# Kernel optimization log

Measured on AMD Instinct MI355X. Metric: run time of the kernel, lower is better.

Reference implementation:

```python
import jax, jax.numpy as jnp
import numpy as np

LN_EPS = 1e-5  # torch LayerNorm default
EPS = 1e-8     # slot-attention eps

def _ln(x, g, b):
    m = jnp.mean(x, axis=-1, keepdims=True)
    v = jnp.mean(jnp.square(x - m), axis=-1, keepdims=True)
    return (x - m) * jax.lax.rsqrt(v + LN_EPS) * g + b

def setup_inputs() -> dict:
    key = jax.random.key(0)
    ks = jax.random.split(key, 16)
    b, d, n_s, h = 131072, 256, 16, 256
    w_scale = d ** -0.5
    return {
        "inputs": jax.random.normal(ks[0], (b, 1, d), jnp.float32),
        "noise": jax.random.normal(ks[1], (n_s, d), jnp.float32),
        "slots_mu": jax.random.normal(ks[2], (1, d), jnp.float32),
        "slots_sigma": jax.random.uniform(ks[3], (1, d), jnp.float32),
        "Wq": jax.random.normal(ks[4], (d, d), jnp.float32) * w_scale,
        "bq": jnp.zeros((d,), jnp.float32),
        "Wk": jax.random.normal(ks[5], (d, d), jnp.float32) * w_scale,
        "bk": jnp.zeros((d,), jnp.float32),
        "Wv": jax.random.normal(ks[6], (d, d), jnp.float32) * w_scale,
        "bv": jnp.zeros((d,), jnp.float32),
        "W_ih": jax.random.normal(ks[7], (3 * d, d), jnp.float32) * w_scale,
        "W_hh": jax.random.normal(ks[8], (3 * d, d), jnp.float32) * w_scale,
        "b_ih": jnp.zeros((3 * d,), jnp.float32),
        "b_hh": jnp.zeros((3 * d,), jnp.float32),
        "W1": jax.random.normal(ks[9], (h, d), jnp.float32) * w_scale,
        "b1": jnp.zeros((h,), jnp.float32),
        "W2": jax.random.normal(ks[10], (d, h), jnp.float32) * (h ** -0.5),
        "b2": jnp.zeros((d,), jnp.float32),
        "g_in": jnp.ones((d,), jnp.float32),
        "be_in": jnp.zeros((d,), jnp.float32),
        "g_s": jnp.ones((d,), jnp.float32),
        "be_s": jnp.zeros((d,), jnp.float32),
        "g_f": jnp.ones((d,), jnp.float32),
        "be_f": jnp.zeros((d,), jnp.float32),
    }

def reference(inputs, noise, slots_mu, slots_sigma, Wq, bq, Wk, bk, Wv, bv,
              W_ih, W_hh, b_ih, b_hh, W1, b1, W2, b2,
              g_in, be_in, g_s, be_s, g_f, be_f):
    b, w, d = inputs.shape  # w == 1 required by the module's LayerNorm(dim)
    x = inputs.reshape(b, w * d)
    scale = d ** -0.5
    iters = 3

    slots = slots_mu + slots_sigma * noise  # (n_s, d), reparameterized normal

    x = _ln(x, g_in, be_in)
    k = x @ Wk.T + bk  # (b, d)
    v = x @ Wv.T + bv  # (b, d)

    for _ in range(iters):
        slots_prev = slots
        s = _ln(slots, g_s, be_s)
        q = s @ Wq.T + bq                      # (n_s, d)
        dots = jnp.einsum('nd,bd->nb', q, k) * scale
        attn = jax.nn.softmax(dots, axis=0) + EPS   # softmax over slots
        attn = attn / jnp.sum(attn, axis=-1, keepdims=True)
        updates = jnp.einsum('bd,nb->nd', v, attn)  # (n_s, d)
        # torch GRUCell
        gx = updates @ W_ih.T + b_ih                # (n_s, 3d)
        gh = slots_prev @ W_hh.T + b_hh
        xr, xz, xn = jnp.split(gx, 3, axis=-1)
        hr, hz, hn = jnp.split(gh, 3, axis=-1)
        r = jax.nn.sigmoid(xr + hr)
        z = jax.nn.sigmoid(xz + hz)
        n = jnp.tanh(xn + r * hn)
        slots = (1.0 - z) * n + z * slots_prev
        ff = jax.nn.relu(_ln(slots, g_f, be_f) @ W1.T + b1) @ W2.T + b2
        slots = slots + ff
    return slots
```

## Files before the change

### kernel.cpp

```cpp
#include <hip/hip_runtime.h>
#include <stdint.h>

#define B_ROWS 131072
#define SCALE 0.0625f
#define LN_EPS 1e-5f
#define ATTN_EPS 1e-8f

#define BIG_BLOCKS 512
#define ROWS_PER_BLOCK (B_ROWS / BIG_BLOCKS)
#define ROWS_PER_WAVE  (ROWS_PER_BLOCK / 4)
#define NSLICE BIG_BLOCKS

#define WS_PARTU 0
#define WS_PARTS (WS_PARTU + NSLICE*4096)
#define WS_U     (WS_PARTS + NSLICE*16)
#define WS_S     (WS_U + 4096)
#define WS_SLOTS (WS_S + 64)
#define WS_MID   (WS_SLOTS + 4096)
#define WS_GX    (WS_MID + 4096)
#define WS_GH    (WS_GX + 12288)
#define WS_H1    (WS_GH + 12288)
#define WS_QKG   (WS_H1 + 4096)
#define WS_QB    (WS_QKG + 4096)
#define WS_WIHV  (WS_QB + 64)
#define WS_BGX   (WS_WIHV + 196608)
#define WS_WQKG  (WS_BGX + 768)
#define WS_U2G   (WS_WQKG + 65536)
#define WS_U1    (WS_U2G + 256)
#define WS_C1    (WS_U1 + 256)

__global__ __launch_bounds__(256) void k_pre1(
    const float* __restrict__ Wq, const float* __restrict__ bq,
    const float* __restrict__ Wk, const float* __restrict__ bk,
    const float* __restrict__ Wv, const float* __restrict__ bv,
    const float* __restrict__ W_ih, const float* __restrict__ b_ih,
    const float* __restrict__ g_in, const float* __restrict__ be_in,
    float* __restrict__ ws)
{
  int bid = blockIdx.x, t = threadIdx.x;
  if (bid < 48) {
    int j0 = bid * 16;
    float acc[16];
#pragma unroll
    for (int r = 0; r < 16; r++) acc[r] = 0.f;
    int d = t;
    for (int dd = 0; dd < 256; dd++) {
      float v = Wv[dd * 256 + d];
#pragma unroll
      for (int r = 0; r < 16; r++)
        acc[r] = fmaf(W_ih[(j0 + r) * 256 + dd], v, acc[r]);
    }
#pragma unroll
    for (int r = 0; r < 16; r++) ws[WS_WIHV + (j0 + r) * 256 + d] = acc[r];
    if (t < 16) {
      int j = j0 + t;
      float a = b_ih[j];
      for (int dd = 0; dd < 256; dd++)
        a = fmaf(W_ih[j * 256 + dd], bv[dd], a);
      ws[WS_BGX + j] = a;
    }
  } else if (bid < 80) {
    int c0 = (bid - 48) * 8;
    float acc[8];
#pragma unroll
    for (int r = 0; r < 8; r++) acc[r] = 0.f;
    int d = t;
    for (int i = 0; i < 256; i++) {
      float wq = Wq[i * 256 + d];
#pragma unroll
      for (int r = 0; r < 8; r++)
        acc[r] = fmaf(wq, Wk[i * 256 + c0 + r], acc[r]);
    }
#pragma unroll
    for (int r = 0; r < 8; r++) {
      float gc = g_in[c0 + r];
      ws[WS_WQKG + (c0 + r) * 256 + d] = SCALE * gc * acc[r];
    }
    if (t < 8) {
      int c = c0 + t;
      float a = 0.f;
      for (int i = 0; i < 256; i++)
        a = fmaf(bq[i], Wk[i * 256 + c], a);
      ws[WS_U2G + c] = SCALE * g_in[c] * a;
    }
  } else {
    __shared__ __align__(16) float t2[256];
    int j = t;
    float a = 0.f;
    for (int dp = 0; dp < 256; dp++)
      a = fmaf(Wk[j * 256 + dp], be_in[dp], a);
    t2[j] = a + bk[j];
    __syncthreads();
    int d = t;
    float u = 0.f;
    for (int i = 0; i < 256; i++)
      u = fmaf(Wq[i * 256 + d], t2[i], u);
    ws[WS_U1 + d] = u;
    if (t == 0) {
      float c = 0.f;
      for (int i = 0; i < 256; i++) c = fmaf(bq[i], t2[i], c);
      ws[WS_C1] = c;
    }
  }
}

__global__ __launch_bounds__(256) void k_qkg(
    const float* __restrict__ noise, const float* __restrict__ mu,
    const float* __restrict__ sigma, const float* __restrict__ g_s,
    const float* __restrict__ be_s, float* __restrict__ ws, int init)
{
  __shared__ __align__(16) float sS[16 * 260];
  __shared__ __align__(16) float sAux[512];
  __shared__ __align__(16) float sStat[32];
  int bid = blockIdx.x, t = threadIdx.x;
  for (int n = 0; n < 16; n++) {
    float v;
    if (init) v = fmaf(sigma[t], noise[n * 256 + t], mu[t]);
    else      v = ws[WS_SLOTS + n * 256 + t];
    sS[n * 260 + t] = v;
    if (init && bid == 0) ws[WS_SLOTS + n * 256 + t] = v;
  }
  __syncthreads();
  { int n = t >> 4, c = t & 15;
    float s1 = 0.f, s2 = 0.f;
    for (int k = 0; k < 16; k++) {
      float x = sS[n * 260 + c * 16 + k];
      s1 += x; s2 = fmaf(x, x, s2);
    }
    sAux[n * 16 + c] = s1; sAux[256 + n * 16 + c] = s2; }
  __syncthreads();
  if (t < 16) {
    float s1 = 0.f, s2 = 0.f;
    for (int c = 0; c < 16; c++) { s1 += sAux[t * 16 + c]; s2 += sAux[256 + t * 16 + c]; }
    float m = s1 * (1.f / 256.f);
    float v = fmaxf(fmaf(-m, m, s2 * (1.f / 256.f)), 0.f);
    sStat[t] = m; sStat[16 + t] = rsqrtf(v + LN_EPS);
  }
  __syncthreads();
  { float gs = g_s[t], bs = be_s[t];
    for (int n = 0; n < 16; n++) {
      float m = sStat[n], rs = sStat[16 + n];
      sS[n * 260 + t] = fmaf((sS[n * 260 + t] - m) * rs, gs, bs);
    } }
  __syncthreads();
  if (bid < 64) {
    int cr = t >> 6, n = (t >> 2) & 15, ks = t & 3;
    int c = bid * 4 + cr;
    const float* wrow = ws + WS_WQKG + c * 256 + ks * 64;
    const float* srow = &sS[n * 260 + ks * 64];
    float acc = 0.f;
#pragma unroll
    for (int i = 0; i < 16; i++) {
      float4 w = *(const float4*)(wrow + i * 4);
      float4 s4 = *(const float4*)(srow + i * 4);
      acc = fmaf(w.x, s4.x, fmaf(w.y, s4.y, fmaf(w.z, s4.z, fmaf(w.w, s4.w, acc))));
    }
    sAux[t] = acc;
    __syncthreads();
    if (t < 64) {
      int cr2 = t >> 4, n2 = t & 15;
      int c2 = bid * 4 + cr2;
      int b = cr2 * 64 + n2 * 4;
      float s = sAux[b] + sAux[b + 1] + sAux[b + 2] + sAux[b + 3];
      ws[WS_QKG + n2 * 256 + c2] = s + ws[WS_U2G + c2];
    }
  } else {
    int n = t >> 4, ks = t & 15;
    float acc = 0.f;
    for (int k = 0; k < 16; k++)
      acc = fmaf(sS[n * 260 + ks * 16 + k], ws[WS_U1 + ks * 16 + k], acc);
    sAux[t] = acc;
    __syncthreads();
    if (t < 16) {
      float s = 0.f;
      for (int k = 0; k < 16; k++) s += sAux[t * 16 + k];
      ws[WS_QB + t] = SCALE * (s + ws[WS_C1]);
    }
  }
}

__global__ __launch_bounds__(256, 2) void k_big(
    const float* __restrict__ X, float* __restrict__ ws)
{
  __shared__ __align__(16) float red[4 * 4096];
  __shared__ __align__(16) float redS[64];
  int t = threadIdx.x;
  int wave = t >> 6, lane = t & 63;
  int p = lane >> 4, g = lane & 15;

  const float* qkg = ws + WS_QKG;
  float qw[4][16];
  float qs[4];
#pragma unroll
  for (int i = 0; i < 4; i++) {
    const float* rp = qkg + (4 * p + i) * 256 + g * 16;
#pragma unroll
    for (int jq = 0; jq < 4; jq++) {
      float4 v4 = *(const float4*)(rp + 4 * jq);
      qw[i][4 * jq + 0] = v4.x; qw[i][4 * jq + 1] = v4.y;
      qw[i][4 * jq + 2] = v4.z; qw[i][4 * jq + 3] = v4.w;
    }
    float s = 0.f;
#pragma unroll
    for (int j = 0; j < 16; j++) s += qw[i][j];
    qs[i] = s;
  }
#pragma unroll
  for (int m = 1; m <= 8; m <<= 1) {
#pragma unroll
    for (int i = 0; i < 4; i++) qs[i] += __shfl_xor(qs[i], m);
  }
  float qb0[4];
  {
    float4 q4 = *(const float4*)(ws + WS_QB + 4 * p);
    qb0[0] = q4.x; qb0[1] = q4.y; qb0[2] = q4.z; qb0[3] = q4.w;
  }

  float P[4][16];
#pragma unroll
  for (int i = 0; i < 4; i++)
#pragma unroll
    for (int j = 0; j < 16; j++) P[i][j] = 0.f;
  float Q[4] = {0.f, 0.f, 0.f, 0.f};
  float Sa[4] = {0.f, 0.f, 0.f, 0.f};

  size_t rowbase = (size_t)blockIdx.x * ROWS_PER_BLOCK + (size_t)wave * ROWS_PER_WAVE;
  const float* cur = X + rowbase * 256 + g * 16;
  float4 va = *(const float4*)cur;
  float4 vb = *(const float4*)(cur + 4);
  float4 vc = *(const float4*)(cur + 8);
  float4 vd = *(const float4*)(cur + 12);

#pragma unroll 1
  for (int r = 0; r < ROWS_PER_WAVE; r++) {
    const float* nxt = (r < ROWS_PER_WAVE - 1) ? (cur + 256) : cur;
    float4 na = *(const float4*)nxt;
    float4 nb = *(const float4*)(nxt + 4);
    float4 nc = *(const float4*)(nxt + 8);
    float4 nd = *(const float4*)(nxt + 12);

    float x[16];
    x[0] = va.x; x[1] = va.y; x[2] = va.z; x[3] = va.w;
    x[4] = vb.x; x[5] = vb.y; x[6] = vb.z; x[7] = vb.w;
    x[8] = vc.x; x[9] = vc.y; x[10] = vc.z; x[11] = vc.w;
    x[12] = vd.x; x[13] = vd.y; x[14] = vd.z; x[15] = vd.w;

    float s1 = 0.f, s2 = 0.f;
#pragma unroll
    for (int j = 0; j < 16; j++) { s1 += x[j]; s2 = fmaf(x[j], x[j], s2); }
#pragma unroll
    for (int m = 1; m <= 8; m <<= 1) {
      s1 += __shfl_xor(s1, m);
      s2 += __shfl_xor(s2, m);
    }
    float mean = s1 * (1.f / 256.f);
    float var = fmaxf(fmaf(-mean, mean, s2 * (1.f / 256.f)), 0.f);
    float rs = rsqrtf(var + LN_EPS);
    float mrs = mean * rs;

    float d0 = 0.f, d1 = 0.f, d2 = 0.f, d3 = 0.f;
#pragma unroll
    for (int j = 0; j < 16; j++) {
      d0 = fmaf(qw[0][j], x[j], d0);
      d1 = fmaf(qw[1][j], x[j], d1);
      d2 = fmaf(qw[2][j], x[j], d2);
      d3 = fmaf(qw[3][j], x[j], d3);
    }
#pragma unroll
    for (int m = 1; m <= 8; m <<= 1) {
      d0 += __shfl_xor(d0, m); d1 += __shfl_xor(d1, m);
      d2 += __shfl_xor(d2, m); d3 += __shfl_xor(d3, m);
    }
    float dsc[4];
    dsc[0] = fmaf(rs, d0, fmaf(-mrs, qs[0], qb0[0]));
    dsc[1] = fmaf(rs, d1, fmaf(-mrs, qs[1], qb0[1]));
    dsc[2] = fmaf(rs, d2, fmaf(-mrs, qs[2], qb0[2]));
    dsc[3] = fmaf(rs, d3, fmaf(-mrs, qs[3], qb0[3]));

    float mx = fmaxf(fmaxf(dsc[0], dsc[1]), fmaxf(dsc[2], dsc[3]));
    mx = fmaxf(mx, __shfl_xor(mx, 16));
    mx = fmaxf(mx, __shfl_xor(mx, 32));
    float e[4];
#pragma unroll
    for (int i = 0; i < 4; i++) e[i] = __expf(dsc[i] - mx);
    float se = e[0] + e[1] + e[2] + e[3];
    se += __shfl_xor(se, 16);
    se += __shfl_xor(se, 32);
    float inv = 1.0f / se;
    float a0[4], ar[4];
#pragma unroll
    for (int i = 0; i < 4; i++) {
      a0[i] = fmaf(e[i], inv, ATTN_EPS);
      ar[i] = a0[i] * rs;
    }
#pragma unroll
    for (int j = 0; j < 16; j++) {
      P[0][j] = fmaf(ar[0], x[j], P[0][j]);
      P[1][j] = fmaf(ar[1], x[j], P[1][j]);
      P[2][j] = fmaf(ar[2], x[j], P[2][j]);
      P[3][j] = fmaf(ar[3], x[j], P[3][j]);
    }
#pragma unroll
    for (int i = 0; i < 4; i++) {
      Q[i] = fmaf(a0[i], mrs, Q[i]);
      Sa[i] += a0[i];
    }
    va = na; vb = nb; vc = nc; vd = nd; cur = nxt;
  }

  if (g == 0) {
#pragma unroll
    for (int i = 0; i < 4; i++) redS[wave * 16 + 4 * p + i] = Sa[i];
  }
#pragma unroll
  for (int i = 0; i < 4; i++) {
#pragma unroll
    for (int jq = 0; jq < 4; jq++) {
      float4 v4;
      v4.x = P[i][4 * jq + 0] - Q[i]; v4.y = P[i][4 * jq + 1] - Q[i];
      v4.z = P[i][4 * jq + 2] - Q[i]; v4.w = P[i][4 * jq + 3] - Q[i];
      *(float4*)&red[wave * 4096 + (4 * p + i) * 256 + g * 16 + jq * 4] = v4;
    }
  }
  __syncthreads();
#pragma unroll
  for (int k = 0; k < 16; k++) {
    int idx = k * 256 + t;
    float v = red[idx] + red[4096 + idx] + red[8192 + idx] + red[12288 + idx];
    ws[WS_PARTU + (size_t)blockIdx.x * 4096 + idx] = v;
  }
  if (t < 16) {
    float sv = redS[t] + redS[16 + t] + redS[32 + t] + redS[48 + t];
    ws[WS_PARTS + blockIdx.x * 16 + t] = sv;
  }
}

__global__ __launch_bounds__(256) void k_red(float* __restrict__ ws)
{
  __shared__ __align__(16) float sAux[256];
  int bid = blockIdx.x, t = threadIdx.x;
  if (bid < 256) {
    int el = t & 15, wg = t >> 4;
    int e = bid * 16 + el;
    float acc = 0.f;
#pragma unroll 8
    for (int k = 0; k < 32; k++)
      acc += ws[WS_PARTU + (size_t)(wg + k * 16) * 4096 + e];
    sAux[t] = acc;
    __syncthreads();
    if (t < 16) {
      float s = 0.f;
      for (int w = 0; w < 16; w++) s += sAux[w * 16 + t];
      ws[WS_U + bid * 16 + t] = s;
    }
  } else {
    int n = t & 15, wg = t >> 4;
    float acc = 0.f;
#pragma unroll 8
    for (int k = 0; k < 32; k++)
      acc += ws[WS_PARTS + (wg + k * 16) * 16 + n];
    sAux[t] = acc;
    __syncthreads();
    if (t < 16) {
      float s = 0.f;
      for (int w = 0; w < 16; w++) s += sAux[w * 16 + t];
      ws[WS_S + t] = s;
    }
  }
}

__global__ __launch_bounds__(256) void k_gxgh(
    const float* __restrict__ W_hh, const float* __restrict__ b_hh,
    const float* __restrict__ g_in, const float* __restrict__ be_in,
    float* __restrict__ ws)
{
  __shared__ __align__(16) float sU[16 * 260];
  __shared__ __align__(16) float sInv[16];
  int bid = blockIdx.x, t = threadIdx.x;
  bool isgx = bid < 64;
  if (isgx && t < 16) sInv[t] = 1.0f / ws[WS_S + t];
  __syncthreads();
  if (isgx) {
    float gi = g_in[t], bi = be_in[t];
    for (int n = 0; n < 16; n++)
      sU[n * 260 + t] = fmaf(gi * ws[WS_U + n * 256 + t], sInv[n], bi);
  } else {
    for (int n = 0; n < 16; n++)
      sU[n * 260 + t] = ws[WS_SLOTS + n * 256 + t];
  }
  __syncthreads();
  int jr = t >> 4, n = t & 15;
  if (jr < 12) {
    int j = (isgx ? bid : bid - 64) * 12 + jr;
    const float* srow = &sU[n * 260];
    const float* wrow = isgx ? (ws + WS_WIHV + j * 256) : (W_hh + j * 256);
    float acc = isgx ? ws[WS_BGX + j] : b_hh[j];
#pragma unroll 8
    for (int k = 0; k < 64; k++) {
      float4 w = *(const float4*)(wrow + k * 4);
      float4 s4 = *(const float4*)(srow + k * 4);
      acc = fmaf(w.x, s4.x, fmaf(w.y, s4.y, fmaf(w.z, s4.z, fmaf(w.w, s4.w, acc))));
    }
    if (isgx) ws[WS_GX + n * 768 + j] = acc;
    else      ws[WS_GH + n * 768 + j] = acc;
  }
}

__global__ __launch_bounds__(256) void k_midh1(
    const float* __restrict__ W1, const float* __restrict__ b1,
    const float* __restrict__ g_f, const float* __restrict__ be_f,
    float* __restrict__ ws)
{
  __shared__ __align__(16) float sM[16 * 260];
  __shared__ __align__(16) float sAux[512];
  __shared__ __align__(16) float sStat[32];
  int bid = blockIdx.x, t = threadIdx.x;
  for (int n = 0; n < 16; n++) {
    float xr = ws[WS_GX + n * 768 + t],       hr = ws[WS_GH + n * 768 + t];
    float xz = ws[WS_GX + n * 768 + 256 + t], hz = ws[WS_GH + n * 768 + 256 + t];
    float xn = ws[WS_GX + n * 768 + 512 + t], hn = ws[WS_GH + n * 768 + 512 + t];
    float sp = ws[WS_SLOTS + n * 256 + t];
    float r = 1.f / (1.f + __expf(-(xr + hr)));
    float z = 1.f / (1.f + __expf(-(xz + hz)));
    float nn = tanhf(fmaf(r, hn, xn));
    float mid = fmaf(z, sp - nn, nn);
    sM[n * 260 + t] = mid;
    if (bid == 0) ws[WS_MID + n * 256 + t] = mid;
  }
  __syncthreads();
  { int n = t >> 4, c = t & 15;
    float s1 = 0.f, s2 = 0.f;
    for (int k = 0; k < 16; k++) {
      float x = sM[n * 260 + c * 16 + k];
      s1 += x; s2 = fmaf(x, x, s2);
    }
    sAux[n * 16 + c] = s1; sAux[256 + n * 16 + c] = s2; }
  __syncthreads();
  if (t < 16) {
    float s1 = 0.f, s2 = 0.f;
    for (int c = 0; c < 16; c++) { s1 += sAux[t * 16 + c]; s2 += sAux[256 + t * 16 + c]; }
    float m = s1 * (1.f / 256.f);
    float v = fmaxf(fmaf(-m, m, s2 * (1.f / 256.f)), 0.f);
    sStat[t] = m; sStat[16 + t] = rsqrtf(v + LN_EPS);
  }
  __syncthreads();
  { float gf = g_f[t], bf = be_f[t];
    for (int n = 0; n < 16; n++) {
      float m = sStat[n], rs = sStat[16 + n];
      sM[n * 260 + t] = fmaf((sM[n * 260 + t] - m) * rs, gf, bf);
    } }
  __syncthreads();
  int jr = t >> 6, n = (t >> 2) & 15, ks = t & 3;
  int j = bid * 4 + jr;
  const float* wrow = W1 + j * 256 + ks * 64;
  const float* srow = &sM[n * 260 + ks * 64];
  float acc = 0.f;
#pragma unroll
  for (int k = 0; k < 16; k++) {
    float4 w = *(const float4*)(wrow + k * 4);
    float4 s4 = *(const float4*)(srow + k * 4);
    acc = fmaf(w.x, s4.x, fmaf(w.y, s4.y, fmaf(w.z, s4.z, fmaf(w.w, s4.w, acc))));
  }
  sAux[t] = acc;
  __syncthreads();
  if (t < 64) {
    int jr2 = t >> 4, n2 = t & 15;
    int j2 = bid * 4 + jr2;
    int b = jr2 * 64 + n2 * 4;
    float s = sAux[b] + sAux[b + 1] + sAux[b + 2] + sAux[b + 3] + b1[j2];
    ws[WS_H1 + n2 * 256 + j2] = fmaxf(s, 0.f);
  }
}

__global__ __launch_bounds__(256) void k_ffnew(
    const float* __restrict__ W2, const float* __restrict__ b2v,
    float* __restrict__ out, float* __restrict__ ws)
{
  __shared__ __align__(16) float sH[16 * 260];
  __shared__ __align__(16) float sAux[256];
  int bid = blockIdx.x, t = threadIdx.x;
  for (int n = 0; n < 16; n++)
    sH[n * 260 + t] = ws[WS_H1 + n * 256 + t];
  __syncthreads();
  int dr = t >> 6, n = (t >> 2) & 15, ks = t & 3;
  int d = bid * 4 + dr;
  const float* wrow = W2 + d * 256 + ks * 64;
  const float* srow = &sH[n * 260 + ks * 64];
  float acc = 0.f;
#pragma unroll
  for (int k = 0; k < 16; k++) {
    float4 w = *(const float4*)(wrow + k * 4);
    float4 s4 = *(const float4*)(srow + k * 4);
    acc = fmaf(w.x, s4.x, fmaf(w.y, s4.y, fmaf(w.z, s4.z, fmaf(w.w, s4.w, acc))));
  }
  sAux[t] = acc;
  __syncthreads();
  if (t < 64) {
    int dr2 = t >> 4, n2 = t & 15;
    int d2 = bid * 4 + dr2;
    int b = dr2 * 64 + n2 * 4;
    float s = sAux[b] + sAux[b + 1] + sAux[b + 2] + sAux[b + 3]
            + b2v[d2] + ws[WS_MID + n2 * 256 + d2];
    ws[WS_SLOTS + n2 * 256 + d2] = s;
    out[n2 * 256 + d2] = s;
  }
}

extern "C" void kernel_launch(void* const* d_in, const int* in_sizes, int n_in,
                              void* d_out, int out_size, void* d_ws, size_t ws_size,
                              hipStream_t stream)
{
  (void)in_sizes; (void)n_in; (void)out_size; (void)ws_size;
  const float* inputs = (const float*)d_in[0];
  const float* noise  = (const float*)d_in[1];
  const float* mu     = (const float*)d_in[2];
  const float* sigma  = (const float*)d_in[3];
  const float* Wq     = (const float*)d_in[4];
  const float* bq     = (const float*)d_in[5];
  const float* Wk     = (const float*)d_in[6];
  const float* bk     = (const float*)d_in[7];
  const float* Wv     = (const float*)d_in[8];
  const float* bv     = (const float*)d_in[9];
  const float* W_ih   = (const float*)d_in[10];
  const float* W_hh   = (const float*)d_in[11];
  const float* b_ih   = (const float*)d_in[12];
  const float* b_hh   = (const float*)d_in[13];
  const float* W1     = (const float*)d_in[14];
  const float* b1     = (const float*)d_in[15];
  const float* W2     = (const float*)d_in[16];
  const float* b2     = (const float*)d_in[17];
  const float* g_in   = (const float*)d_in[18];
  const float* be_in  = (const float*)d_in[19];
  const float* g_s    = (const float*)d_in[20];
  const float* be_s   = (const float*)d_in[21];
  const float* g_f    = (const float*)d_in[22];
  const float* be_f   = (const float*)d_in[23];
  float* ws = (float*)d_ws;
  float* out = (float*)d_out;

  hipLaunchKernelGGL(k_pre1, dim3(81), dim3(256), 0, stream,
                     Wq, bq, Wk, bk, Wv, bv, W_ih, b_ih, g_in, be_in, ws);
  hipLaunchKernelGGL(k_qkg, dim3(65), dim3(256), 0, stream,
                     noise, mu, sigma, g_s, be_s, ws, 1);
  for (int it = 0; it < 3; it++) {
    hipLaunchKernelGGL(k_big, dim3(BIG_BLOCKS), dim3(256), 0, stream, inputs, ws);
    hipLaunchKernelGGL(k_red, dim3(257), dim3(256), 0, stream, ws);
    hipLaunchKernelGGL(k_gxgh, dim3(128), dim3(256), 0, stream,
                       W_hh, b_hh, g_in, be_in, ws);
    hipLaunchKernelGGL(k_midh1, dim3(64), dim3(256), 0, stream,
                       W1, b1, g_f, be_f, ws);
    hipLaunchKernelGGL(k_ffnew, dim3(64), dim3(256), 0, stream,
                       W2, b2, out, ws);
    if (it < 2)
      hipLaunchKernelGGL(k_qkg, dim3(65), dim3(256), 0, stream,
                         noise, mu, sigma, g_s, be_s, ws, 0);
  }
}
```

Baseline: 653.0 us.

## Replace partial-sum buffer and reduction kernel with global atomics in k_big

k_big no longer writes per-block partial sums for a separate k_red kernel to combine. Each block now reduces its four waves into a smaller shared buffer, one wave at a time, and then atomically adds the result into the global accumulators. Those accumulators are zeroed by an extra block in k_qkg before each k_big runs. The block count is doubled and the launch bound raised to four blocks per CU to increase occupancy. The aim is to drop one launch per iteration and the round trip of the partial buffer, at the cost of heavy atomic contention on 4096 addresses, extra barriers, and possible register spills.

```diff
diff --git a/kernel.cpp b/kernel.cpp
--- a/kernel.cpp
+++ b/kernel.cpp
@@ -6,28 +6,25 @@
 #define LN_EPS 1e-5f
 #define ATTN_EPS 1e-8f
 
-#define BIG_BLOCKS 512
+#define BIG_BLOCKS 1024
 #define ROWS_PER_BLOCK (B_ROWS / BIG_BLOCKS)
 #define ROWS_PER_WAVE  (ROWS_PER_BLOCK / 4)
-#define NSLICE BIG_BLOCKS
-
-#define WS_PARTU 0
-#define WS_PARTS (WS_PARTU + NSLICE*4096)
-#define WS_U     (WS_PARTS + NSLICE*16)
-#define WS_S     (WS_U + 4096)
-#define WS_SLOTS (WS_S + 64)
-#define WS_MID   (WS_SLOTS + 4096)
-#define WS_GX    (WS_MID + 4096)
-#define WS_GH    (WS_GX + 12288)
-#define WS_H1    (WS_GH + 12288)
-#define WS_QKG   (WS_H1 + 4096)
-#define WS_QB    (WS_QKG + 4096)
-#define WS_WIHV  (WS_QB + 64)
-#define WS_BGX   (WS_WIHV + 196608)
-#define WS_WQKG  (WS_BGX + 768)
-#define WS_U2G   (WS_WQKG + 65536)
-#define WS_U1    (WS_U2G + 256)
-#define WS_C1    (WS_U1 + 256)
+
+#define WS_U     0
+#define WS_S     4096
+#define WS_SLOTS 4160
+#define WS_MID   8256
+#define WS_GX    12352
+#define WS_GH    24640
+#define WS_H1    36928
+#define WS_QKG   41024
+#define WS_QB    45120
+#define WS_WIHV  45184
+#define WS_BGX   241792
+#define WS_WQKG  242560
+#define WS_U2G   308096
+#define WS_U1    308352
+#define WS_C1    308608
 
 __global__ __launch_bounds__(256) void k_pre1(
     const float* __restrict__ Wq, const float* __restrict__ bq,
@@ -113,6 +110,11 @@
   __shared__ __align__(16) float sAux[512];
   __shared__ __align__(16) float sStat[32];
   int bid = blockIdx.x, t = threadIdx.x;
+  if (bid == 64) {
+#pragma unroll
+    for (int k = 0; k < 16; k++) ws[WS_U + k * 256 + t] = 0.f;
+    if (t < 16) ws[WS_S + t] = 0.f;
+  }
   for (int n = 0; n < 16; n++) {
     float v;
     if (init) v = fmaf(sigma[t], noise[n * 256 + t], mu[t]);
@@ -179,10 +181,10 @@
   }
 }
 
-__global__ __launch_bounds__(256, 2) void k_big(
+__global__ __launch_bounds__(256, 4) void k_big(
     const float* __restrict__ X, float* __restrict__ ws)
 {
-  __shared__ __align__(16) float red[4 * 4096];
+  __shared__ __align__(16) float red[16 * 256];
   __shared__ __align__(16) float redS[64];
   int t = threadIdx.x;
   int wave = t >> 6, lane = t & 63;
@@ -312,60 +314,38 @@
 #pragma unroll
     for (int i = 0; i < 4; i++) redS[wave * 16 + 4 * p + i] = Sa[i];
   }
-#pragma unroll
-  for (int i = 0; i < 4; i++) {
-#pragma unroll
-    for (int jq = 0; jq < 4; jq++) {
-      float4 v4;
-      v4.x = P[i][4 * jq + 0] - Q[i]; v4.y = P[i][4 * jq + 1] - Q[i];
-      v4.z = P[i][4 * jq + 2] - Q[i]; v4.w = P[i][4 * jq + 3] - Q[i];
-      *(float4*)&red[wave * 4096 + (4 * p + i) * 256 + g * 16 + jq * 4] = v4;
+#pragma unroll 1
+  for (int w = 0; w < 4; w++) {
+    if (w) __syncthreads();
+    if (wave == w) {
+#pragma unroll
+      for (int i = 0; i < 4; i++) {
+#pragma unroll
+        for (int jq = 0; jq < 4; jq++) {
+          int idx = (4 * p + i) * 256 + g * 16 + jq * 4;
+          float4 v4;
+          v4.x = P[i][4 * jq + 0] - Q[i]; v4.y = P[i][4 * jq + 1] - Q[i];
+          v4.z = P[i][4 * jq + 2] - Q[i]; v4.w = P[i][4 * jq + 3] - Q[i];
+          if (w == 0) {
+            *(float4*)&red[idx] = v4;
+          } else {
+            float4 o = *(const float4*)&red[idx];
+            v4.x += o.x; v4.y += o.y; v4.z += o.z; v4.w += o.w;
+            *(float4*)&red[idx] = v4;
+          }
+        }
+      }
     }
   }
   __syncthreads();
 #pragma unroll
   for (int k = 0; k < 16; k++) {
     int idx = k * 256 + t;
-    float v = red[idx] + red[4096 + idx] + red[8192 + idx] + red[12288 + idx];
-    ws[WS_PARTU + (size_t)blockIdx.x * 4096 + idx] = v;
+    atomicAdd(&ws[WS_U + idx], red[idx]);
   }
   if (t < 16) {
     float sv = redS[t] + redS[16 + t] + redS[32 + t] + redS[48 + t];
-    ws[WS_PARTS + blockIdx.x * 16 + t] = sv;
-  }
-}
-
-__global__ __launch_bounds__(256) void k_red(float* __restrict__ ws)
-{
-  __shared__ __align__(16) float sAux[256];
-  int bid = blockIdx.x, t = threadIdx.x;
-  if (bid < 256) {
-    int el = t & 15, wg = t >> 4;
-    int e = bid * 16 + el;
-    float acc = 0.f;
-#pragma unroll 8
-    for (int k = 0; k < 32; k++)
-      acc += ws[WS_PARTU + (size_t)(wg + k * 16) * 4096 + e];
-    sAux[t] = acc;
-    __syncthreads();
-    if (t < 16) {
-      float s = 0.f;
-      for (int w = 0; w < 16; w++) s += sAux[w * 16 + t];
-      ws[WS_U + bid * 16 + t] = s;
-    }
-  } else {
-    int n = t & 15, wg = t >> 4;
-    float acc = 0.f;
-#pragma unroll 8
-    for (int k = 0; k < 32; k++)
-      acc += ws[WS_PARTS + (wg + k * 16) * 16 + n];
-    sAux[t] = acc;
-    __syncthreads();
-    if (t < 16) {
-      float s = 0.f;
-      for (int w = 0; w < 16; w++) s += sAux[w * 16 + t];
-      ws[WS_S + t] = s;
-    }
+    atomicAdd(&ws[WS_S + t], sv);
   }
 }
 
@@ -544,7 +524,6 @@
                      noise, mu, sigma, g_s, be_s, ws, 1);
   for (int it = 0; it < 3; it++) {
     hipLaunchKernelGGL(k_big, dim3(BIG_BLOCKS), dim3(256), 0, stream, inputs, ws);
-    hipLaunchKernelGGL(k_red, dim3(257), dim3(256), 0, stream, ws);
     hipLaunchKernelGGL(k_gxgh, dim3(128), dim3(256), 0, stream,
                        W_hh, b_hh, g_in, be_in, ws);
     hipLaunchKernelGGL(k_midh1, dim3(64), dim3(256), 0, stream,
```

Result: slower. 1.274 ms (+95.1%).
